# Optimization experiments

Hardware: AMD Instinct MI355X
Metric: run time of the kernel (lower is better)

Reference implementation:

```python
import jax, jax.numpy as jnp
import numpy as np

B, S, D_IN, D_OUT, H = 2, 2048, 1024, 1024, 16
DH = D_OUT // H

def setup_inputs() -> dict:
    key = jax.random.key(0)
    ks = jax.random.split(key, 6)
    sc = 0.02
    return {
        'x': jax.random.normal(ks[0], (B, S, D_IN), dtype=jnp.float32),
        'Wq': jax.random.normal(ks[1], (D_IN, D_OUT), dtype=jnp.float32) * sc,
        'Wk': jax.random.normal(ks[2], (D_IN, D_OUT), dtype=jnp.float32) * sc,
        'Wv': jax.random.normal(ks[3], (D_IN, D_OUT), dtype=jnp.float32) * sc,
        'Wo': jax.random.normal(ks[4], (D_OUT, D_OUT), dtype=jnp.float32) * sc,
        'bo': jax.random.normal(ks[5], (D_OUT,), dtype=jnp.float32) * sc,
    }

def reference(x, Wq, Wk, Wv, Wo, bo):
    b, s, _ = x.shape
    # projections, split heads: (b, h, s, dh)
    q = (x @ Wq).reshape(b, s, H, DH).transpose(0, 2, 1, 3)
    k = (x @ Wk).reshape(b, s, H, DH).transpose(0, 2, 1, 3)
    v = (x @ Wv).reshape(b, s, H, DH).transpose(0, 2, 1, 3)
    scores = jnp.einsum('bhqd,bhkd->bhqk', q, k)
    causal = jnp.triu(jnp.ones((s, s), dtype=bool), k=1)
    scores = jnp.where(causal, -jnp.inf, scores)
    attn = jax.nn.softmax(scores / jnp.sqrt(jnp.float32(DH)), axis=-1)
    ctx = jnp.einsum('bhqk,bhkd->bhqd', attn, v)
    ctx = ctx.transpose(0, 2, 1, 3).reshape(b, s, D_OUT)
    return ctx @ Wo + bo
```

## Files before the change

### kernel.cpp

```cpp
#include <hip/hip_runtime.h>
#include <hip/hip_bf16.h>
#include <cstdint>

typedef __attribute__((ext_vector_type(8))) __bf16 bf16x8;
typedef __attribute__((ext_vector_type(4))) float f32x4;
typedef __attribute__((ext_vector_type(8))) unsigned short u16x8;
typedef __attribute__((ext_vector_type(4))) unsigned short u16x4;
typedef __attribute__((ext_vector_type(4))) unsigned int u32x4;

#define NEG_INF (-__builtin_inff())

__device__ __forceinline__ unsigned short f2bf(float f) {
    unsigned int u = __builtin_bit_cast(unsigned int, f);
    u += 0x7FFFu + ((u >> 16) & 1u);
    return (unsigned short)(u >> 16);
}
__device__ __forceinline__ float bf2f(unsigned short u) {
    return __builtin_bit_cast(float, (unsigned int)u << 16);
}

__device__ __forceinline__ void gload16(const void* g, void* l) {
    __builtin_amdgcn_global_load_lds(
        (__attribute__((address_space(1))) void*)(uintptr_t)g,
        (__attribute__((address_space(3))) void*)(uint32_t)(uintptr_t)l, 16, 0, 0);
}

__global__ void prep_kernel(const float* __restrict__ x, const float* __restrict__ W0,
                            const float* __restrict__ W1, const float* __restrict__ W2,
                            const float* __restrict__ W3, unsigned short* __restrict__ xb,
                            unsigned short* __restrict__ Wcat, unsigned short* __restrict__ Wot) {
    __shared__ float t[32][33];
    const int z = blockIdx.z;
    if (z == 4) {
        size_t i = ((size_t)(blockIdx.y * 32 + blockIdx.x) * 256 + threadIdx.x) * 2;
        #pragma unroll
        for (int v = 0; v < 2; ++v) {
            const float4* p = (const float4*)x + (i + v) * 2;
            float4 a = p[0], c = p[1];
            u16x8 o;
            o[0] = f2bf(a.x); o[1] = f2bf(a.y); o[2] = f2bf(a.z); o[3] = f2bf(a.w);
            o[4] = f2bf(c.x); o[5] = f2bf(c.y); o[6] = f2bf(c.z); o[7] = f2bf(c.w);
            ((u16x8*)xb)[i + v] = o;
        }
        return;
    }
    const float* src = (z == 0) ? W0 : (z == 1) ? W1 : (z == 2) ? W2 : W3;
    unsigned short* dst = (z < 3) ? (Wcat + (size_t)z * 1024 * 1024) : Wot;
    int n0 = blockIdx.x * 32, k0 = blockIdx.y * 32;
    int tx = threadIdx.x & 31, ty = threadIdx.x >> 5;
    #pragma unroll
    for (int i = 0; i < 4; ++i) {
        int r = ty + i * 8;
        t[r][tx] = src[(size_t)(k0 + r) * 1024 + n0 + tx];
    }
    __syncthreads();
    #pragma unroll
    for (int i = 0; i < 4; ++i) {
        int r = ty + i * 8;
        dst[(size_t)(n0 + r) * 1024 + k0 + tx] = f2bf(t[tx][r]);
    }
}

__global__ __launch_bounds__(256, 2)
void gemm_qkv_kernel(const unsigned short* __restrict__ A, const unsigned short* __restrict__ Bt,
                     unsigned short* __restrict__ Qb, unsigned short* __restrict__ Kb,
                     unsigned short* __restrict__ Vtb) {
    __shared__ unsigned short As[128 * 64];
    __shared__ unsigned short Bs[128 * 64];
    const int tid = threadIdx.x;
    const int w = tid >> 6, l = tid & 63;
    const int lr = l & 15, lg = l >> 4;
    const int wr = w >> 1, wc = w & 1;
    const int id = blockIdx.y * 24 + blockIdx.x;
    const int swz = (id & 7) * 96 + (id >> 3);
    const int m0 = (swz / 24) * 128;
    const int n0 = (swz % 24) * 128;
    const int K = 1024;

    f32x4 acc[4][4] = {};

    for (int k0 = 0; k0 < 1024; k0 += 64) {
        #pragma unroll
        for (int p = 0; p < 4; ++p) {
            int seg = p * 4 + w;
            int row = seg * 8 + (l >> 3);
            int c16 = (l & 7) ^ (row & 7);
            gload16(A  + (size_t)(m0 + row) * K + k0 + c16 * 8, &As[seg * 512]);
            gload16(Bt + (size_t)(n0 + row) * K + k0 + c16 * 8, &Bs[seg * 512]);
        }
        __syncthreads();
        #pragma unroll
        for (int ks = 0; ks < 2; ++ks) {
            bf16x8 af[4], bfr[4];
            #pragma unroll
            for (int i = 0; i < 4; ++i) {
                int ra = wr * 64 + i * 16 + lr;
                af[i] = *(const bf16x8*)&As[ra * 64 + (((ks << 2) | lg) ^ (ra & 7)) * 8];
                int rb = wc * 64 + i * 16 + lr;
                bfr[i] = *(const bf16x8*)&Bs[rb * 64 + (((ks << 2) | lg) ^ (rb & 7)) * 8];
            }
            #pragma unroll
            for (int i = 0; i < 4; ++i)
                #pragma unroll
                for (int j = 0; j < 4; ++j)
                    acc[i][j] = __builtin_amdgcn_mfma_f32_16x16x32_bf16(af[i], bfr[j], acc[i][j], 0, 0, 0);
        }
        __syncthreads();
    }

    const int seg = n0 >> 10;
    const int n0l = n0 & 1023;
    if (seg < 2) {
        unsigned short* C = (seg == 0) ? Qb : Kb;
        const float sc = (seg == 0) ? 0.125f * 1.44269504f : 1.0f;
        #pragma unroll
        for (int i = 0; i < 4; ++i)
            #pragma unroll
            for (int j = 0; j < 4; ++j) {
                int n = n0l + wc * 64 + j * 16 + lr;
                #pragma unroll
                for (int r = 0; r < 4; ++r) {
                    int m = m0 + wr * 64 + i * 16 + lg * 4 + r;
                    C[(size_t)m * 1024 + n] = f2bf(acc[i][j][r] * sc);
                }
            }
    } else {
        #pragma unroll
        for (int i = 0; i < 4; ++i)
            #pragma unroll
            for (int j = 0; j < 4; ++j) {
                int n = n0l + wc * 64 + j * 16 + lr;
                int mb = m0 + wr * 64 + i * 16 + lg * 4;
                int bb = mb >> 11, s = mb & 2047;
                int s6 = s & 63;
                int kp = (((s6 >> 4) & 1) << 5) | (((s6 >> 2) & 3) << 3) | (((s6 >> 5) & 1) << 2);
                int sp = (s & ~63) | kp;
                u16x4 o;
                #pragma unroll
                for (int r = 0; r < 4; ++r) o[r] = f2bf(acc[i][j][r]);
                *(u16x4*)&Vtb[((size_t)(bb * 1024 + n)) * 2048 + sp] = o;
            }
    }
}

static __device__ const unsigned char QS_TAB[24] = {
    7,15,14,14,13,6,12,5,
    15,13,12,10,11,10,11,9,
    0,1,2,3,8,8,9,4};
static __device__ const unsigned char TY_TAB[24] = {
    0,2,1,2,2,0,2,0,
    1,1,1,1,1,2,2,2,
    0,0,0,0,1,2,1,0};

__global__ __launch_bounds__(256, 4)
void flash_attn_kernel(const unsigned short* __restrict__ Q, const unsigned short* __restrict__ Kg,
                       const unsigned short* __restrict__ Vt, unsigned short* __restrict__ ctx,
                       unsigned short* __restrict__ P_O, float* __restrict__ P_l) {
    __shared__ unsigned short Ks[2][4096];
    __shared__ unsigned short Vs[2][4096];
    const int tid = threadIdx.x, w = tid >> 6, l = tid & 63;
    const int lr = l & 15, lg = l >> 4;

    const int level = blockIdx.x >> 5;
    const int bh = blockIdx.x & 31;
    const int qs = QS_TAB[level], ty = TY_TAB[level];
    const int Tf = 2 * qs + 2, mid = qs + 1;
    const int t0 = (ty == 2) ? mid : 0;
    const int t1 = (ty == 1) ? mid : Tf;
    const int b = bh >> 4, h = bh & 15;
    const int qw = qs * 128 + w * 32;

    const int srow8 = w * 8 + (l >> 3);
    const int scol  = (l & 7) ^ (srow8 & 7);
    const unsigned short* Kbase = Kg + (size_t)(b * 2048) * 1024 + h * 64;
    const unsigned short* Vbase = Vt + (size_t)(b * 1024 + h * 64) * 2048;

    const __bf16 one = (__bf16)1.0f;
    const bf16x8 ones = {one, one, one, one, one, one, one, one};

    bf16x8 qf[2][2];
    #pragma unroll
    for (int mi = 0; mi < 2; ++mi)
        #pragma unroll
        for (int ks = 0; ks < 2; ++ks)
            qf[mi][ks] = *(const bf16x8*)&Q[(size_t)(b * 2048 + qw + mi * 16 + lr) * 1024 + h * 64 + ks * 32 + lg * 8];

    f32x4 lacc[2] = {};
    f32x4 oacc[2][4] = {};

    #pragma unroll
    for (int p = 0; p < 2; ++p)
        gload16(Kbase + (size_t)(t0 * 64 + p * 32 + srow8) * 1024 + scol * 8, &Ks[0][(p * 32 + w * 8) * 64]);

    for (int t = t0; t < t1; ++t) {
        const int cur = (t - t0) & 1;
        const int k0 = t * 64;
        #pragma unroll
        for (int p = 0; p < 2; ++p)
            gload16(Vbase + (size_t)(p * 32 + srow8) * 2048 + k0 + scol * 8, &Vs[cur][(p * 32 + w * 8) * 64]);
        const int ktn = (t + 1 < t1) ? t + 1 : t0;
        #pragma unroll
        for (int p = 0; p < 2; ++p)
            gload16(Kbase + (size_t)(ktn * 64 + p * 32 + srow8) * 1024 + scol * 8, &Ks[cur ^ 1][(p * 32 + w * 8) * 64]);

        asm volatile("s_waitcnt vmcnt(4)" ::: "memory");
        __builtin_amdgcn_s_barrier();

        f32x4 sf[2][4] = {};
        __builtin_amdgcn_s_setprio(1);
        #pragma unroll
        for (int ks = 0; ks < 2; ++ks) {
            bf16x8 kf[4];
            #pragma unroll
            for (int ni = 0; ni < 4; ++ni) {
                int rk = ni * 16 + lr;
                kf[ni] = *(const bf16x8*)&Ks[cur][rk * 64 + (((ks << 2) | lg) ^ (rk & 7)) * 8];
            }
            #pragma unroll
            for (int ni = 0; ni < 4; ++ni)
                #pragma unroll
                for (int mi = 0; mi < 2; ++mi)
                    sf[mi][ni] = __builtin_amdgcn_mfma_f32_16x16x32_bf16(kf[ni], qf[mi][ks], sf[mi][ni], 0, 0, 0);
        }
        __builtin_amdgcn_s_setprio(0);

        u32x4 pa0u[2], pa1u[2];
        #pragma unroll
        for (int mi = 0; mi < 2; ++mi) {
            if (t >= Tf - 2) {
                #pragma unroll
                for (int ni = 0; ni < 4; ++ni)
                    #pragma unroll
                    for (int r = 0; r < 4; ++r)
                        if (k0 + ni * 16 + lg * 4 + r > qw + mi * 16 + lr) sf[mi][ni][r] = NEG_INF;
            }
            #pragma unroll
            for (int ni = 0; ni < 4; ++ni)
                #pragma unroll
                for (int r = 0; r < 4; ++r)
                    sf[mi][ni][r] = __builtin_amdgcn_exp2f(sf[mi][ni][r]);

            asm("v_cvt_pk_bf16_f32 %0, %1, %2" : "=v"(pa0u[mi][0]) : "v"(sf[mi][0][0]), "v"(sf[mi][0][1]));
            asm("v_cvt_pk_bf16_f32 %0, %1, %2" : "=v"(pa0u[mi][1]) : "v"(sf[mi][0][2]), "v"(sf[mi][0][3]));
            asm("v_cvt_pk_bf16_f32 %0, %1, %2" : "=v"(pa0u[mi][2]) : "v"(sf[mi][2][0]), "v"(sf[mi][2][1]));
            asm("v_cvt_pk_bf16_f32 %0, %1, %2" : "=v"(pa0u[mi][3]) : "v"(sf[mi][2][2]), "v"(sf[mi][2][3]));
            asm("v_cvt_pk_bf16_f32 %0, %1, %2" : "=v"(pa1u[mi][0]) : "v"(sf[mi][1][0]), "v"(sf[mi][1][1]));
            asm("v_cvt_pk_bf16_f32 %0, %1, %2" : "=v"(pa1u[mi][1]) : "v"(sf[mi][1][2]), "v"(sf[mi][1][3]));
            asm("v_cvt_pk_bf16_f32 %0, %1, %2" : "=v"(pa1u[mi][2]) : "v"(sf[mi][3][0]), "v"(sf[mi][3][1]));
            asm("v_cvt_pk_bf16_f32 %0, %1, %2" : "=v"(pa1u[mi][3]) : "v"(sf[mi][3][2]), "v"(sf[mi][3][3]));

            lacc[mi] = __builtin_amdgcn_mfma_f32_16x16x32_bf16(
                __builtin_bit_cast(bf16x8, pa0u[mi]), ones, lacc[mi], 0, 0, 0);
            lacc[mi] = __builtin_amdgcn_mfma_f32_16x16x32_bf16(
                __builtin_bit_cast(bf16x8, pa1u[mi]), ones, lacc[mi], 0, 0, 0);
        }

        asm volatile("s_waitcnt vmcnt(2)" ::: "memory");
        __builtin_amdgcn_s_barrier();

        __builtin_amdgcn_s_setprio(1);
        #pragma unroll
        for (int ks = 0; ks < 2; ++ks) {
            bf16x8 vb[4];
            #pragma unroll
            for (int ni = 0; ni < 4; ++ni) {
                int rv = ni * 16 + lr;
                vb[ni] = *(const bf16x8*)&Vs[cur][rv * 64 + (((ks << 2) | lg) ^ (rv & 7)) * 8];
            }
            #pragma unroll
            for (int mi = 0; mi < 2; ++mi) {
                bf16x8 pa = __builtin_bit_cast(bf16x8, ks ? pa1u[mi] : pa0u[mi]);
                #pragma unroll
                for (int ni = 0; ni < 4; ++ni)
                    oacc[mi][ni] = __builtin_amdgcn_mfma_f32_16x16x32_bf16(pa, vb[ni], oacc[mi][ni], 0, 0, 0);
            }
        }
        __builtin_amdgcn_s_setprio(0);
    }

    if (ty == 0) {
        #pragma unroll
        for (int mi = 0; mi < 2; ++mi)
            #pragma unroll
            for (int r = 0; r < 4; ++r) {
                float inv = 1.0f / lacc[mi][r];
                int q = qw + mi * 16 + lg * 4 + r;
                size_t base = (size_t)(b * 2048 + q) * 1024 + h * 64 + lr;
                #pragma unroll
                for (int ni = 0; ni < 4; ++ni)
                    ctx[base + ni * 16] = f2bf(oacc[mi][ni][r] * inv);
            }
    } else {
        const int pidx = ((qs - 8) * 32 + bh) * 2 + (ty - 1);
        unsigned short* po = P_O + (size_t)pidx * 8192;
        #pragma unroll
        for (int mi = 0; mi < 2; ++mi)
            #pragma unroll
            for (int r = 0; r < 4; ++r) {
                int rowl = w * 32 + mi * 16 + lg * 4 + r;
                #pragma unroll
                for (int ni = 0; ni < 4; ++ni)
                    po[rowl * 64 + ni * 16 + lr] = f2bf(oacc[mi][ni][r]);
            }
        if (lr == 0) {
            #pragma unroll
            for (int mi = 0; mi < 2; ++mi)
                #pragma unroll
                for (int r = 0; r < 4; ++r)
                    P_l[pidx * 128 + w * 32 + mi * 16 + lg * 4 + r] = lacc[mi][r];
        }
    }
}

__global__ __launch_bounds__(256)
void combine_kernel(const unsigned short* __restrict__ P_O, const float* __restrict__ P_l,
                    unsigned short* __restrict__ ctx) {
    const int qs = 8 + (blockIdx.x >> 5);
    const int bh = blockIdx.x & 31;
    const int b = bh >> 4, h = bh & 15;
    const int p0 = ((qs - 8) * 32 + bh) * 2, p1 = p0 + 1;
    const int t = threadIdx.x;
    const int row = t >> 1, half = t & 1;
    const float inv = 1.0f / (P_l[p0 * 128 + row] + P_l[p1 * 128 + row]);
    const u16x8* o0 = (const u16x8*)&P_O[(size_t)p0 * 8192 + row * 64 + half * 32];
    const u16x8* o1 = (const u16x8*)&P_O[(size_t)p1 * 8192 + row * 64 + half * 32];
    unsigned short* dst = ctx + (size_t)(b * 2048 + qs * 128 + row) * 1024 + h * 64 + half * 32;
    #pragma unroll
    for (int v = 0; v < 4; ++v) {
        u16x8 a = o0[v], c = o1[v], o;
        #pragma unroll
        for (int j = 0; j < 8; ++j)
            o[j] = f2bf((bf2f(a[j]) + bf2f(c[j])) * inv);
        ((u16x8*)dst)[v] = o;
    }
}

__global__ __launch_bounds__(256, 4)
void gemm_out_kernel(const unsigned short* __restrict__ A, const unsigned short* __restrict__ Bt,
                     float* __restrict__ C, const float* __restrict__ bias) {
    __shared__ unsigned short As[128 * 64];
    __shared__ unsigned short Bs[64 * 64];
    const int tid = threadIdx.x;
    const int w = tid >> 6, l = tid & 63;
    const int lr = l & 15, lg = l >> 4;
    const int wr = w >> 1, wc = w & 1;
    const int id = blockIdx.y * 16 + blockIdx.x;
    const int swz = (id & 7) * 64 + (id >> 3);
    const int m0 = (swz >> 4) * 128;
    const int n0 = (swz & 15) * 64;
    const int K = 1024;

    f32x4 acc[4][2] = {};

    for (int k0 = 0; k0 < 1024; k0 += 64) {
        #pragma unroll
        for (int p = 0; p < 4; ++p) {
            int seg = p * 4 + w;
            int row = seg * 8 + (l >> 3);
            int c16 = (l & 7) ^ (row & 7);
            gload16(A + (size_t)(m0 + row) * K + k0 + c16 * 8, &As[seg * 512]);
        }
        #pragma unroll
        for (int p = 0; p < 2; ++p) {
            int seg = p * 4 + w;
            int row = seg * 8 + (l >> 3);
            int c16 = (l & 7) ^ (row & 7);
            gload16(Bt + (size_t)(n0 + row) * K + k0 + c16 * 8, &Bs[seg * 512]);
        }
        __syncthreads();
        #pragma unroll
        for (int ks = 0; ks < 2; ++ks) {
            bf16x8 af[4], bfr[2];
            #pragma unroll
            for (int i = 0; i < 4; ++i) {
                int ra = wr * 64 + i * 16 + lr;
                af[i] = *(const bf16x8*)&As[ra * 64 + (((ks << 2) | lg) ^ (ra & 7)) * 8];
            }
            #pragma unroll
            for (int j = 0; j < 2; ++j) {
                int rb = wc * 32 + j * 16 + lr;
                bfr[j] = *(const bf16x8*)&Bs[rb * 64 + (((ks << 2) | lg) ^ (rb & 7)) * 8];
            }
            #pragma unroll
            for (int i = 0; i < 4; ++i)
                #pragma unroll
                for (int j = 0; j < 2; ++j)
                    acc[i][j] = __builtin_amdgcn_mfma_f32_16x16x32_bf16(af[i], bfr[j], acc[i][j], 0, 0, 0);
        }
        __syncthreads();
    }

    #pragma unroll
    for (int i = 0; i < 4; ++i)
        #pragma unroll
        for (int j = 0; j < 2; ++j) {
            int n = n0 + wc * 32 + j * 16 + lr;
            float bv = bias[n];
            #pragma unroll
            for (int r = 0; r < 4; ++r) {
                int m = m0 + wr * 64 + i * 16 + lg * 4 + r;
                C[(size_t)m * 1024 + n] = acc[i][j][r] + bv;
            }
        }
}

extern "C" void kernel_launch(void* const* d_in, const int* in_sizes, int n_in,
                              void* d_out, int out_size, void* d_ws, size_t ws_size,
                              hipStream_t stream) {
    (void)in_sizes; (void)n_in; (void)out_size; (void)ws_size;
    const float* x  = (const float*)d_in[0];
    const float* Wq = (const float*)d_in[1];
    const float* Wk = (const float*)d_in[2];
    const float* Wv = (const float*)d_in[3];
    const float* Wo = (const float*)d_in[4];
    const float* bo = (const float*)d_in[5];
    float* out = (float*)d_out;

    char* ws = (char*)d_ws;
    const size_t MB = 1024 * 1024;
    unsigned short* xb   = (unsigned short*)(ws);
    unsigned short* Wcat = (unsigned short*)(ws + 8  * MB);
    unsigned short* Wot  = (unsigned short*)(ws + 14 * MB);
    unsigned short* Qb   = (unsigned short*)(ws + 16 * MB);
    unsigned short* Kb   = (unsigned short*)(ws + 24 * MB);
    unsigned short* Vtb  = (unsigned short*)(ws + 32 * MB);
    unsigned short* Cxb  = (unsigned short*)(ws + 40 * MB);

    unsigned short* P_O  = (unsigned short*)(ws);
    float*          P_l  = (float*)(ws + 8 * MB);

    prep_kernel<<<dim3(32, 32, 5), 256, 0, stream>>>(x, Wq, Wk, Wv, Wo, xb, Wcat, Wot);
    gemm_qkv_kernel<<<dim3(24, 32), 256, 0, stream>>>(xb, Wcat, Qb, Kb, Vtb);
    flash_attn_kernel<<<768, 256, 0, stream>>>(Qb, Kb, Vtb, Cxb, P_O, P_l);
    combine_kernel<<<256, 256, 0, stream>>>(P_O, P_l, Cxb);
    gemm_out_kernel<<<dim3(16, 32), 256, 0, stream>>>(Cxb, Wot, out, bo);
}
```

Measured before the change: 86.12 us.

## Enlarge QKV GEMM tile to 256x256 with double-buffered LDS prefetch

The QKV projection GEMM moves from 128x128 tiles with 4 waves to 256x256 tiles with 8 waves (512 threads), launched as 192 blocks instead of 768. LDS is double-buffered so the next K-slice is fetched while MFMAs run on the current one, with one barrier per iteration and raised wave priority around the MFMA block. The goal is more operand reuse per global load and hidden load latency. In exchange, 192 blocks may underfill the GPU's CUs, and the larger register and LDS footprint cuts occupancy to one block.

```diff
diff --git a/kernel.cpp b/kernel.cpp
--- a/kernel.cpp
+++ b/kernel.cpp
@@ -61,51 +61,85 @@
     }
 }
 
-__global__ __launch_bounds__(256, 2)
+__global__ __launch_bounds__(512, 1)
 void gemm_qkv_kernel(const unsigned short* __restrict__ A, const unsigned short* __restrict__ Bt,
                      unsigned short* __restrict__ Qb, unsigned short* __restrict__ Kb,
                      unsigned short* __restrict__ Vtb) {
-    __shared__ unsigned short As[128 * 64];
-    __shared__ unsigned short Bs[128 * 64];
+    __shared__ unsigned short As[2][16384];
+    __shared__ unsigned short Bs[2][16384];
     const int tid = threadIdx.x;
     const int w = tid >> 6, l = tid & 63;
     const int lr = l & 15, lg = l >> 4;
-    const int wr = w >> 1, wc = w & 1;
-    const int id = blockIdx.y * 24 + blockIdx.x;
-    const int swz = (id & 7) * 96 + (id >> 3);
-    const int m0 = (swz / 24) * 128;
-    const int n0 = (swz % 24) * 128;
+    const int wr = w >> 2, wc = w & 3;
+    const int id = blockIdx.x;
+    const int swz = (id & 7) * 24 + (id >> 3);
+    const int m0 = (swz / 12) * 256;
+    const int n0 = (swz % 12) * 256;
     const int K = 1024;
 
-    f32x4 acc[4][4] = {};
-
-    for (int k0 = 0; k0 < 1024; k0 += 64) {
-        #pragma unroll
-        for (int p = 0; p < 4; ++p) {
-            int seg = p * 4 + w;
-            int row = seg * 8 + (l >> 3);
-            int c16 = (l & 7) ^ (row & 7);
-            gload16(A  + (size_t)(m0 + row) * K + k0 + c16 * 8, &As[seg * 512]);
-            gload16(Bt + (size_t)(n0 + row) * K + k0 + c16 * 8, &Bs[seg * 512]);
-        }
-        __syncthreads();
-        #pragma unroll
-        for (int ks = 0; ks < 2; ++ks) {
-            bf16x8 af[4], bfr[4];
-            #pragma unroll
-            for (int i = 0; i < 4; ++i) {
-                int ra = wr * 64 + i * 16 + lr;
-                af[i] = *(const bf16x8*)&As[ra * 64 + (((ks << 2) | lg) ^ (ra & 7)) * 8];
-                int rb = wc * 64 + i * 16 + lr;
-                bfr[i] = *(const bf16x8*)&Bs[rb * 64 + (((ks << 2) | lg) ^ (rb & 7)) * 8];
-            }
-            #pragma unroll
-            for (int i = 0; i < 4; ++i)
+    const int srow_base = (l >> 3);
+    const int sc8 = l & 7;
+
+    f32x4 acc[8][4] = {};
+
+    #pragma unroll
+    for (int p = 0; p < 4; ++p) {
+        int seg = p * 8 + w;
+        int row = seg * 8 + srow_base;
+        int c16 = sc8 ^ (row & 7);
+        gload16(A  + (size_t)(m0 + row) * K + c16 * 8, &As[0][seg * 512]);
+        gload16(Bt + (size_t)(n0 + row) * K + c16 * 8, &Bs[0][seg * 512]);
+    }
+    asm volatile("s_waitcnt vmcnt(0)" ::: "memory");
+    __builtin_amdgcn_s_barrier();
+
+    for (int t = 0; t < 16; ++t) {
+        const int cb = t & 1, nb = cb ^ 1;
+        const int k0n = (t + 1) * 64;
+        const bool pf = (t + 1 < 16);
+
+        bf16x8 bfr[4][2];
+        #pragma unroll
+        for (int j = 0; j < 4; ++j) {
+            int rb = wc * 64 + j * 16 + lr;
+            #pragma unroll
+            for (int ks = 0; ks < 2; ++ks)
+                bfr[j][ks] = *(const bf16x8*)&Bs[cb][rb * 64 + (((ks << 2) | lg) ^ (rb & 7)) * 8];
+        }
+
+        #pragma unroll
+        for (int qd = 0; qd < 4; ++qd) {
+            if (pf) {
+                int seg = qd * 8 + w;
+                int row = seg * 8 + srow_base;
+                int c16 = sc8 ^ (row & 7);
+                gload16(A  + (size_t)(m0 + row) * K + k0n + c16 * 8, &As[nb][seg * 512]);
+                gload16(Bt + (size_t)(n0 + row) * K + k0n + c16 * 8, &Bs[nb][seg * 512]);
+            }
+            bf16x8 af[2][2];
+            #pragma unroll
+            for (int e = 0; e < 2; ++e) {
+                int ra = wr * 128 + (qd * 2 + e) * 16 + lr;
+                #pragma unroll
+                for (int ks = 0; ks < 2; ++ks)
+                    af[e][ks] = *(const bf16x8*)&As[cb][ra * 64 + (((ks << 2) | lg) ^ (ra & 7)) * 8];
+            }
+            __builtin_amdgcn_s_setprio(1);
+            #pragma unroll
+            for (int e = 0; e < 2; ++e)
                 #pragma unroll
                 for (int j = 0; j < 4; ++j)
-                    acc[i][j] = __builtin_amdgcn_mfma_f32_16x16x32_bf16(af[i], bfr[j], acc[i][j], 0, 0, 0);
-        }
-        __syncthreads();
+                    #pragma unroll
+                    for (int ks = 0; ks < 2; ++ks)
+                        acc[qd * 2 + e][j] = __builtin_amdgcn_mfma_f32_16x16x32_bf16(
+                            af[e][ks], bfr[j][ks], acc[qd * 2 + e][j], 0, 0, 0);
+            __builtin_amdgcn_s_setprio(0);
+        }
+
+        if (t < 15) {
+            asm volatile("s_waitcnt vmcnt(0)" ::: "memory");
+            __builtin_amdgcn_s_barrier();
+        }
     }
 
     const int seg = n0 >> 10;
@@ -114,30 +148,30 @@
         unsigned short* C = (seg == 0) ? Qb : Kb;
         const float sc = (seg == 0) ? 0.125f * 1.44269504f : 1.0f;
         #pragma unroll
-        for (int i = 0; i < 4; ++i)
+        for (int mi = 0; mi < 8; ++mi)
             #pragma unroll
             for (int j = 0; j < 4; ++j) {
                 int n = n0l + wc * 64 + j * 16 + lr;
                 #pragma unroll
                 for (int r = 0; r < 4; ++r) {
-                    int m = m0 + wr * 64 + i * 16 + lg * 4 + r;
-                    C[(size_t)m * 1024 + n] = f2bf(acc[i][j][r] * sc);
+                    int m = m0 + wr * 128 + mi * 16 + lg * 4 + r;
+                    C[(size_t)m * 1024 + n] = f2bf(acc[mi][j][r] * sc);
                 }
             }
     } else {
         #pragma unroll
-        for (int i = 0; i < 4; ++i)
+        for (int mi = 0; mi < 8; ++mi)
             #pragma unroll
             for (int j = 0; j < 4; ++j) {
                 int n = n0l + wc * 64 + j * 16 + lr;
-                int mb = m0 + wr * 64 + i * 16 + lg * 4;
+                int mb = m0 + wr * 128 + mi * 16 + lg * 4;
                 int bb = mb >> 11, s = mb & 2047;
                 int s6 = s & 63;
                 int kp = (((s6 >> 4) & 1) << 5) | (((s6 >> 2) & 3) << 3) | (((s6 >> 5) & 1) << 2);
                 int sp = (s & ~63) | kp;
                 u16x4 o;
                 #pragma unroll
-                for (int r = 0; r < 4; ++r) o[r] = f2bf(acc[i][j][r]);
+                for (int r = 0; r < 4; ++r) o[r] = f2bf(acc[mi][j][r]);
                 *(u16x4*)&Vtb[((size_t)(bb * 1024 + n)) * 2048 + sp] = o;
             }
     }
@@ -430,7 +464,7 @@
     float*          P_l  = (float*)(ws + 8 * MB);
 
     prep_kernel<<<dim3(32, 32, 5), 256, 0, stream>>>(x, Wq, Wk, Wv, Wo, xb, Wcat, Wot);
-    gemm_qkv_kernel<<<dim3(24, 32), 256, 0, stream>>>(xb, Wcat, Qb, Kb, Vtb);
+    gemm_qkv_kernel<<<192, 512, 0, stream>>>(xb, Wcat, Qb, Kb, Vtb);
     flash_attn_kernel<<<768, 256, 0, stream>>>(Qb, Kb, Vtb, Cxb, P_O, P_l);
     combine_kernel<<<256, 256, 0, stream>>>(P_O, P_l, Cxb);
     gemm_out_kernel<<<dim3(16, 32), 256, 0, stream>>>(Cxb, Wot, out, bo);
```

Result: slower. 89.21 us (+3.6%).
